# Kernel optimization log

Hardware: AMD Instinct MI355X
Metric: run time of the kernel (lower is better)

The kernel has to match this reference:

```python
import jax, jax.numpy as jnp
import numpy as np

EPS = 1e-6  # F.pairwise_distance default eps, added to the difference


def setup_inputs() -> dict:
    key = jax.random.key(0)
    k1, k2 = jax.random.split(key)
    N, NS, NQ, D = 2048, 5, 8, 256
    x = jax.random.normal(k1, (N, NS + NQ, D), dtype=jnp.float32)
    label = jax.random.randint(k2, (N,), 0, N, dtype=jnp.int64)
    return {"x": x, "label": label, "n_s": NS, "n_q": NQ}


def reference(x, label, n_s, n_q):
    # x: [N, n_s+n_q, D]
    anchors = jnp.mean(x[:, :n_s, :], axis=1)               # [N, D] prototypes
    N, D = anchors.shape
    queries = x[:, n_s:n_s + n_q, :].reshape(N * n_q, D)     # [N*n_q, D]

    # Exact ||q - a + eps||^2 via GEMM expansion (matches F.pairwise_distance(.,.)**2):
    # ||q-a||^2 + 2*eps*sum(q-a) + D*eps^2
    q_sq = jnp.sum(queries * queries, axis=-1)               # [N*n_q]
    a_sq = jnp.sum(anchors * anchors, axis=-1)               # [N]
    cross = queries @ anchors.T                              # [N*n_q, N]
    q_sum = jnp.sum(queries, axis=-1)                        # [N*n_q]
    a_sum = jnp.sum(anchors, axis=-1)                        # [N]
    dist_sq = (q_sq[:, None] + a_sq[None, :] - 2.0 * cross
               + 2.0 * EPS * (q_sum[:, None] - a_sum[None, :])
               + D * EPS * EPS)
    logits = -dist_sq                                        # [N*n_q, N]

    lab = jnp.repeat(label, n_q)                             # [N*n_q]
    logp = jax.nn.log_softmax(logits, axis=-1)
    nloss = -jnp.mean(jnp.take_along_axis(logp, lab[:, None], axis=1))
    prec1 = jnp.mean((jnp.argmax(logits, axis=-1) == lab).astype(jnp.float32)) * 100.0
    return nloss, prec1
```

## Files before the change

### kernel.cpp

```cpp
#include <hip/hip_runtime.h>
#include <math.h>

#define EPS  1e-6f
#define DD   256
#define NSUP 5
#define NQ   8
#define SEQ  13
#define L2E  1.44269504088896f
#define LN2  0.693147180559945f
#define NEP  2048
#define NROW 16384
#define NCOL 2048

typedef short bf16x8 __attribute__((ext_vector_type(8)));
typedef unsigned short u16x4 __attribute__((ext_vector_type(4)));
typedef float f32x4  __attribute__((ext_vector_type(4)));

__device__ __forceinline__ ushort f2bf(float f) {
  union { float f; unsigned u; } v; v.f = f;
  unsigned r = v.u + 0x7FFFu + ((v.u >> 16) & 1u);
  return (ushort)(r >> 16);
}
__device__ __forceinline__ float bf2f(short u) {
  union { unsigned u; float f; } v; v.u = ((unsigned)(unsigned short)u) << 16;
  return v.f;
}

__global__ __launch_bounds__(256) void proto_prep(
    const float* __restrict__ x, float* __restrict__ cb,
    ushort* __restrict__ Asw, ushort* __restrict__ Qsw,
    float* __restrict__ accum, int* __restrict__ fincount) {
  const int tid = threadIdx.x, g = tid >> 6, l = tid & 63;
  const int n = blockIdx.x * 4 + g;
  if (blockIdx.x == 0 && tid == 0) { accum[0] = 0.f; accum[1] = 0.f; fincount[0] = 0; }

  const float4* xr4 = (const float4*)(x + (size_t)n * SEQ * DD);

  const int d0   = l * 4;
  const int kk   = d0 >> 5, quad = (d0 >> 3) & 3, j = d0 & 7;
  const size_t chunk_d = (size_t)kk * 64 + (size_t)quad * 16;

  float4 a = {0.f, 0.f, 0.f, 0.f};
  #pragma unroll
  for (int s = 0; s < NSUP; ++s) {
    float4 v = xr4[s * 64 + l];
    a.x += v.x; a.y += v.y; a.z += v.z; a.w += v.w;
  }
  a.x *= 0.2f; a.y *= 0.2f; a.z *= 0.2f; a.w *= 0.2f;
  {
    const size_t idx = (((size_t)(n >> 4) * 8) * 64 + chunk_d + (n & 15)) * 8 + j;
    u16x4 o = {f2bf(a.x), f2bf(a.y), f2bf(a.z), f2bf(a.w)};
    *(u16x4*)(Asw + idx) = o;
  }
  float s1 = a.x + a.y + a.z + a.w;
  float s2 = a.x * a.x + a.y * a.y + a.z * a.z + a.w * a.w;
  #pragma unroll
  for (int off = 32; off; off >>= 1) {
    s1 += __shfl_xor(s1, off);
    s2 += __shfl_xor(s2, off);
  }
  if (l == 0) cb[n] = -L2E * (s2 - 2.f * EPS * s1);

  #pragma unroll
  for (int s = 0; s < NQ; ++s) {
    float4 q = xr4[(NSUP + s) * 64 + l];
    const int row = n * NQ + s;
    const size_t idx = (((size_t)(row >> 4) * 8) * 64 + chunk_d + (row & 15)) * 8 + j;
    u16x4 o = {f2bf(q.x), f2bf(q.y), f2bf(q.z), f2bf(q.w)};
    *(u16x4*)(Qsw + idx) = o;
  }
}

__global__ __launch_bounds__(1024, 4) void proto_main(
    const ushort* __restrict__ Qsw, const ushort* __restrict__ Asw,
    const float* __restrict__ cb, const int* __restrict__ label,
    float* __restrict__ accum, int* __restrict__ fincount,
    float* __restrict__ out) {
  const int tid  = threadIdx.x;
  const int wid  = tid >> 6, lane = tid & 63;
  const int quad = lane >> 4, lcol = lane & 15;
  const int rowg = wid & 1, colg = wid >> 1;
  const int r0   = blockIdx.x * 64;

  const bf16x8* qb = (const bf16x8*)Qsw;
  const bf16x8* bb = (const bf16x8*)Asw;

  __shared__ bf16x8 Bl[8][2][8][64];

  bf16x8 af[2][8];
  #pragma unroll
  for (int set = 0; set < 2; ++set) {
    const size_t base = ((size_t)(blockIdx.x * 4 + rowg * 2 + set) * 8) * 64 + lane;
    #pragma unroll
    for (int kk = 0; kk < 8; ++kk) af[set][kk] = qb[base + (size_t)kk * 64];
  }

  float m[2][4], s[2][4];
  int   bi[2][4];
  #pragma unroll
  for (int set = 0; set < 2; ++set)
    #pragma unroll
    for (int i = 0; i < 4; ++i) {
      m[set][i] = -1e30f; s[set][i] = 0.f; bi[set][i] = 0x7fffffff;
    }

  const int kk0 = rowg * 4;
  auto stage = [&](int tl, int b) {
    const int T = colg * 16 + tl;
    #pragma unroll
    for (int k2 = 0; k2 < 4; ++k2) {
      const int kk = kk0 + k2;
      const ushort* src = Asw + (((size_t)T * 8 + kk) * 64 + lane) * 8;
      __builtin_amdgcn_global_load_lds(
          (const __attribute__((address_space(1))) void*)src,
          (__attribute__((address_space(3))) void*)&Bl[colg][b][kk][0],
          16, 0, 0);
    }
  };

  auto compute = [&](int tl, int b) {
    f32x4 c0 = {0.f, 0.f, 0.f, 0.f}, c1 = {0.f, 0.f, 0.f, 0.f};
    #pragma unroll
    for (int kk = 0; kk < 8; ++kk) {
      bf16x8 bf = Bl[colg][b][kk][lane];
      c0 = __builtin_amdgcn_mfma_f32_16x16x32_bf16(af[0][kk], bf, c0, 0, 0, 0);
      c1 = __builtin_amdgcn_mfma_f32_16x16x32_bf16(af[1][kk], bf, c1, 0, 0, 0);
    }
    const int   colIdx = (colg * 16 + tl) * 16 + lcol;
    const float cbv    = cb[colIdx];
    #pragma unroll
    for (int set = 0; set < 2; ++set) {
      #pragma unroll
      for (int i = 0; i < 4; ++i) {
        float cv = set ? c1[i] : c0[i];
        float v2 = fmaf(cv, 2.f * L2E, cbv);
        float dv = v2 - m[set][i];
        bool  gt = dv > 0.f;
        float e  = exp2f(-fabsf(dv));
        s[set][i]  = fmaf(s[set][i], gt ? e : 1.f, gt ? 1.f : e);
        m[set][i]  = fmaxf(m[set][i], v2);
        bi[set][i] = gt ? colIdx : bi[set][i];
      }
    }
  };

  stage(0, 0);
  __syncthreads();

  #pragma unroll 1
  for (int t = 0; t < 16; t += 2) {
    stage(t + 1, 1);
    compute(t, 0);
    __syncthreads();
    if (t + 2 < 16) stage(t + 2, 0);
    compute(t + 1, 1);
    __syncthreads();
  }

  #pragma unroll
  for (int mask = 1; mask < 16; mask <<= 1) {
    #pragma unroll
    for (int set = 0; set < 2; ++set)
      #pragma unroll
      for (int i = 0; i < 4; ++i) {
        float om = __shfl_xor(m[set][i], mask);
        float os = __shfl_xor(s[set][i], mask);
        int   oi = __shfl_xor(bi[set][i], mask);
        float nm = fmaxf(m[set][i], om);
        s[set][i] = s[set][i] * exp2f(m[set][i] - nm) + os * exp2f(om - nm);
        bool better = (om > m[set][i]) || (om == m[set][i] && oi < bi[set][i]);
        bi[set][i] = better ? oi : bi[set][i];
        m[set][i]  = nm;
      }
  }

  __shared__ float sm[8][64], ssh[8][64], slab[64];
  __shared__ int   sbi[8][64];
  if (lcol == 0) {
    #pragma unroll
    for (int set = 0; set < 2; ++set)
      #pragma unroll
      for (int i = 0; i < 4; ++i) {
        int rl = rowg * 32 + set * 16 + quad * 4 + i;
        sm[colg][rl] = m[set][i]; ssh[colg][rl] = s[set][i]; sbi[colg][rl] = bi[set][i];
      }
  }

  if (tid < 512) {
    const int rl = tid >> 3, l = tid & 7;
    const int row = r0 + rl;
    const int lab = label[row >> 3];
    const int kk  = l;
    float dot = 0.f;
    const size_t qc = ((size_t)(row >> 4) * 8 + kk) * 64 + (row & 15);
    const size_t ac = ((size_t)(lab >> 4) * 8 + kk) * 64 + (lab & 15);
    #pragma unroll
    for (int qd = 0; qd < 4; ++qd) {
      bf16x8 qv = qb[qc + qd * 16];
      bf16x8 av = bb[ac + qd * 16];
      #pragma unroll
      for (int j = 0; j < 8; ++j) dot = fmaf(bf2f(qv[j]), bf2f(av[j]), dot);
    }
    dot += __shfl_xor(dot, 1);
    dot += __shfl_xor(dot, 2);
    dot += __shfl_xor(dot, 4);
    if (l == 0) slab[rl] = fmaf(dot, 2.f * L2E, cb[lab]);
  }
  __syncthreads();

  if (tid < 64) {
    float mm = sm[0][tid], sv = ssh[0][tid];
    int   b  = sbi[0][tid];
    #pragma unroll
    for (int w = 1; w < 8; ++w) {
      float om = sm[w][tid], os = ssh[w][tid];
      int   oi = sbi[w][tid];
      float nm = fmaxf(mm, om);
      sv = sv * exp2f(mm - nm) + os * exp2f(om - nm);
      bool better = (om > mm) || (om == mm && oi < b);
      b = better ? oi : b;
      mm = nm;
    }
    const int row = r0 + tid;
    const int lb  = label[row >> 3];
    float loss = LN2 * (mm + log2f(sv) - slab[tid]);
    float corr = (b == lb) ? 1.f : 0.f;
    #pragma unroll
    for (int mask = 32; mask; mask >>= 1) {
      loss += __shfl_xor(loss, mask);
      corr += __shfl_xor(corr, mask);
    }
    if (tid == 0) {
      atomicAdd(&accum[0], loss);
      atomicAdd(&accum[1], corr);
      __threadfence();
      if (atomicAdd(fincount, 1) == (int)gridDim.x - 1) {
        out[0] = atomicAdd(&accum[0], 0.f) / (float)NROW;
        out[1] = atomicAdd(&accum[1], 0.f) * 100.f / (float)NROW;
      }
    }
  }
}

extern "C" void kernel_launch(void* const* d_in, const int* in_sizes, int n_in,
                              void* d_out, int out_size, void* d_ws, size_t ws_size,
                              hipStream_t stream) {
  const float* x     = (const float*)d_in[0];
  const int*   label = (const int*)d_in[1];
  float* out = (float*)d_out;

  float*  W        = (float*)d_ws;
  float*  accum    = W;
  int*    fincount = (int*)(W + 2);
  float*  cb       = W + 16;
  ushort* Asw      = (ushort*)(cb + NCOL);
  ushort* Qsw      = Asw + (size_t)NCOL * DD;

  hipLaunchKernelGGL(proto_prep, dim3(NEP / 4), dim3(256), 0, stream,
                     x, cb, Asw, Qsw, accum, fincount);
  hipLaunchKernelGGL(proto_main, dim3(NROW / 64), dim3(1024), 0, stream,
                     Qsw, Asw, cb, label, accum, fincount, out);
}
```

Baseline: 121.8 us.

## Software-pipeline MFMA tiles against online softmax and cache column bias in LDS

The per-tile loop is restructured so the MFMA accumulation for tile t runs while the online softmax/argmax update for tile t-1 executes, with two sets of accumulators alternating. The column bias vector is also copied once into shared memory, so the per-tile bias reads come from LDS rather than global memory. This aims to hide the exp/compare latency behind matrix work. In exchange it holds more live accumulator registers and adds 8KB of LDS per block, which could reduce occupancy under the 1024-thread, 4-block launch bound.

```diff
diff --git a/kernel.cpp b/kernel.cpp
--- a/kernel.cpp
+++ b/kernel.cpp
@@ -86,6 +86,10 @@
   const bf16x8* bb = (const bf16x8*)Asw;
 
   __shared__ bf16x8 Bl[8][2][8][64];
+  __shared__ float  sCb[NCOL];
+
+  sCb[tid]        = cb[tid];
+  sCb[tid + 1024] = cb[tid + 1024];
 
   bf16x8 af[2][8];
   #pragma unroll
@@ -118,22 +122,26 @@
     }
   };
 
-  auto compute = [&](int tl, int b) {
-    f32x4 c0 = {0.f, 0.f, 0.f, 0.f}, c1 = {0.f, 0.f, 0.f, 0.f};
+  auto mfmaT = [&](int tl, f32x4 (&c)[2]) {
+    c[0] = f32x4{0.f, 0.f, 0.f, 0.f};
+    c[1] = f32x4{0.f, 0.f, 0.f, 0.f};
+    const int b = tl & 1;
     #pragma unroll
     for (int kk = 0; kk < 8; ++kk) {
       bf16x8 bf = Bl[colg][b][kk][lane];
-      c0 = __builtin_amdgcn_mfma_f32_16x16x32_bf16(af[0][kk], bf, c0, 0, 0, 0);
-      c1 = __builtin_amdgcn_mfma_f32_16x16x32_bf16(af[1][kk], bf, c1, 0, 0, 0);
-    }
+      c[0] = __builtin_amdgcn_mfma_f32_16x16x32_bf16(af[0][kk], bf, c[0], 0, 0, 0);
+      c[1] = __builtin_amdgcn_mfma_f32_16x16x32_bf16(af[1][kk], bf, c[1], 0, 0, 0);
+    }
+  };
+
+  auto smax = [&](int tl, f32x4 (&c)[2]) {
     const int   colIdx = (colg * 16 + tl) * 16 + lcol;
-    const float cbv    = cb[colIdx];
+    const float cbv    = sCb[colIdx];
     #pragma unroll
     for (int set = 0; set < 2; ++set) {
       #pragma unroll
       for (int i = 0; i < 4; ++i) {
-        float cv = set ? c1[i] : c0[i];
-        float v2 = fmaf(cv, 2.f * L2E, cbv);
+        float v2 = fmaf(c[set][i], 2.f * L2E, cbv);
         float dv = v2 - m[set][i];
         bool  gt = dv > 0.f;
         float e  = exp2f(-fabsf(dv));
@@ -144,18 +152,28 @@
     }
   };
 
+  f32x4 cE[2], cO[2];
+
   stage(0, 0);
   __syncthreads();
+  stage(1, 1);
+  mfmaT(0, cE);
+  __syncthreads();
 
   #pragma unroll 1
-  for (int t = 0; t < 16; t += 2) {
-    stage(t + 1, 1);
-    compute(t, 0);
+  for (int t = 1; t < 15; t += 2) {
+    stage(t + 1, 0);
+    mfmaT(t, cO);
+    smax(t - 1, cE);
     __syncthreads();
-    if (t + 2 < 16) stage(t + 2, 0);
-    compute(t + 1, 1);
+    stage(t + 2, 1);
+    mfmaT(t + 1, cE);
+    smax(t, cO);
     __syncthreads();
   }
+  mfmaT(15, cO);
+  smax(14, cE);
+  smax(15, cO);
 
   #pragma unroll
   for (int mask = 1; mask < 16; mask <<= 1) {
@@ -204,7 +222,7 @@
     dot += __shfl_xor(dot, 1);
     dot += __shfl_xor(dot, 2);
     dot += __shfl_xor(dot, 4);
-    if (l == 0) slab[rl] = fmaf(dot, 2.f * L2E, cb[lab]);
+    if (l == 0) slab[rl] = fmaf(dot, 2.f * L2E, sCb[lab]);
   }
   __syncthreads();
 
```

New measurement: 126.7 us. +4.0%, slower.

## Split GEMM columns across two blocks with 128-row tiles and add merge kernel

Applied to the files above, without the earlier changes.

The main kernel now handles 128 query rows per block, with 4 row groups by 4 column groups, and covers half of the 2048 prototype columns. This keeps the grid at 256 blocks while each staged B tile is reused across twice as many rows. Per-half softmax partials (max, sum, argmax) and the label logits are written to workspace, and a new third kernel merges the two halves and reduces loss and accuracy. The column bias is also cached in shared memory. The cost is an extra launch, a global round trip for the partials, and fewer columns per block to amortize the Q fragment loads.

```diff
diff --git a/kernel.cpp b/kernel.cpp
--- a/kernel.cpp
+++ b/kernel.cpp
@@ -74,23 +74,28 @@
 __global__ __launch_bounds__(1024, 4) void proto_main(
     const ushort* __restrict__ Qsw, const ushort* __restrict__ Asw,
     const float* __restrict__ cb, const int* __restrict__ label,
-    float* __restrict__ accum, int* __restrict__ fincount,
-    float* __restrict__ out) {
+    float* __restrict__ partm, float* __restrict__ parts,
+    int* __restrict__ partbi, float* __restrict__ slabws) {
   const int tid  = threadIdx.x;
   const int wid  = tid >> 6, lane = tid & 63;
   const int quad = lane >> 4, lcol = lane & 15;
-  const int rowg = wid & 1, colg = wid >> 1;
-  const int r0   = blockIdx.x * 64;
+  const int rowg = wid & 3, colg = wid >> 2;
+  const int rb   = blockIdx.x >> 1;
+  const int colc = blockIdx.x & 1;
+  const int r0   = rb * 128;
 
   const bf16x8* qb = (const bf16x8*)Qsw;
   const bf16x8* bb = (const bf16x8*)Asw;
 
-  __shared__ bf16x8 Bl[8][2][8][64];
+  __shared__ bf16x8 Bl[4][2][8][64];
+  __shared__ float  sCb[1024];
+
+  sCb[tid] = cb[colc * 1024 + tid];
 
   bf16x8 af[2][8];
   #pragma unroll
   for (int set = 0; set < 2; ++set) {
-    const size_t base = ((size_t)(blockIdx.x * 4 + rowg * 2 + set) * 8) * 64 + lane;
+    const size_t base = ((size_t)(rb * 8 + rowg * 2 + set) * 8) * 64 + lane;
     #pragma unroll
     for (int kk = 0; kk < 8; ++kk) af[set][kk] = qb[base + (size_t)kk * 64];
   }
@@ -104,11 +109,11 @@
       m[set][i] = -1e30f; s[set][i] = 0.f; bi[set][i] = 0x7fffffff;
     }
 
-  const int kk0 = rowg * 4;
+  const int kk0 = rowg * 2;
   auto stage = [&](int tl, int b) {
-    const int T = colg * 16 + tl;
-    #pragma unroll
-    for (int k2 = 0; k2 < 4; ++k2) {
+    const int T = colc * 64 + colg * 16 + tl;
+    #pragma unroll
+    for (int k2 = 0; k2 < 2; ++k2) {
       const int kk = kk0 + k2;
       const ushort* src = Asw + (((size_t)T * 8 + kk) * 64 + lane) * 8;
       __builtin_amdgcn_global_load_lds(
@@ -126,8 +131,9 @@
       c0 = __builtin_amdgcn_mfma_f32_16x16x32_bf16(af[0][kk], bf, c0, 0, 0, 0);
       c1 = __builtin_amdgcn_mfma_f32_16x16x32_bf16(af[1][kk], bf, c1, 0, 0, 0);
     }
-    const int   colIdx = (colg * 16 + tl) * 16 + lcol;
-    const float cbv    = cb[colIdx];
+    const int   lcIdx  = (colg * 16 + tl) * 16 + lcol;
+    const int   colIdx = colc * 1024 + lcIdx;
+    const float cbv    = sCb[lcIdx];
     #pragma unroll
     for (int set = 0; set < 2; ++set) {
       #pragma unroll
@@ -174,8 +180,8 @@
       }
   }
 
-  __shared__ float sm[8][64], ssh[8][64], slab[64];
-  __shared__ int   sbi[8][64];
+  __shared__ float sm[4][128], ssh[4][128];
+  __shared__ int   sbi[4][128];
   if (lcol == 0) {
     #pragma unroll
     for (int set = 0; set < 2; ++set)
@@ -185,8 +191,28 @@
         sm[colg][rl] = m[set][i]; ssh[colg][rl] = s[set][i]; sbi[colg][rl] = bi[set][i];
       }
   }
-
-  if (tid < 512) {
+  __syncthreads();
+
+  if (tid < 128) {
+    float mm = sm[0][tid], sv = ssh[0][tid];
+    int   b  = sbi[0][tid];
+    #pragma unroll
+    for (int w = 1; w < 4; ++w) {
+      float om = sm[w][tid], os = ssh[w][tid];
+      int   oi = sbi[w][tid];
+      float nm = fmaxf(mm, om);
+      sv = sv * exp2f(mm - nm) + os * exp2f(om - nm);
+      bool better = (om > mm) || (om == mm && oi < b);
+      b = better ? oi : b;
+      mm = nm;
+    }
+    const int row = r0 + tid;
+    partm [colc * NROW + row] = mm;
+    parts [colc * NROW + row] = sv;
+    partbi[colc * NROW + row] = b;
+  }
+
+  if (colc == 0) {
     const int rl = tid >> 3, l = tid & 7;
     const int row = r0 + rl;
     const int lab = label[row >> 3];
@@ -204,40 +230,48 @@
     dot += __shfl_xor(dot, 1);
     dot += __shfl_xor(dot, 2);
     dot += __shfl_xor(dot, 4);
-    if (l == 0) slab[rl] = fmaf(dot, 2.f * L2E, cb[lab]);
-  }
+    if (l == 0) slabws[row] = fmaf(dot, 2.f * L2E, cb[lab]);
+  }
+}
+
+__global__ __launch_bounds__(256) void proto_merge(
+    const float* __restrict__ partm, const float* __restrict__ parts,
+    const int* __restrict__ partbi, const float* __restrict__ slabws,
+    const int* __restrict__ label,
+    float* __restrict__ accum, int* __restrict__ fincount,
+    float* __restrict__ out) {
+  const int tid = threadIdx.x, row = blockIdx.x * 256 + tid;
+  const int wid = tid >> 6;
+
+  float m0 = partm[row],  m1 = partm[NROW + row];
+  float s0 = parts[row],  s1 = parts[NROW + row];
+  int   b0 = partbi[row], b1 = partbi[NROW + row];
+  float nm = fmaxf(m0, m1);
+  float sv = s0 * exp2f(m0 - nm) + s1 * exp2f(m1 - nm);
+  bool better = (m1 > m0) || (m1 == m0 && b1 < b0);
+  int  b  = better ? b1 : b0;
+
+  const int lb = label[row >> 3];
+  float loss = LN2 * (nm + log2f(sv) - slabws[row]);
+  float corr = (b == lb) ? 1.f : 0.f;
+
+  #pragma unroll
+  for (int mask = 32; mask; mask >>= 1) {
+    loss += __shfl_xor(loss, mask);
+    corr += __shfl_xor(corr, mask);
+  }
+  __shared__ float red[2][4];
+  if ((tid & 63) == 0) { red[0][wid] = loss; red[1][wid] = corr; }
   __syncthreads();
-
-  if (tid < 64) {
-    float mm = sm[0][tid], sv = ssh[0][tid];
-    int   b  = sbi[0][tid];
-    #pragma unroll
-    for (int w = 1; w < 8; ++w) {
-      float om = sm[w][tid], os = ssh[w][tid];
-      int   oi = sbi[w][tid];
-      float nm = fmaxf(mm, om);
-      sv = sv * exp2f(mm - nm) + os * exp2f(om - nm);
-      bool better = (om > mm) || (om == mm && oi < b);
-      b = better ? oi : b;
-      mm = nm;
-    }
-    const int row = r0 + tid;
-    const int lb  = label[row >> 3];
-    float loss = LN2 * (mm + log2f(sv) - slab[tid]);
-    float corr = (b == lb) ? 1.f : 0.f;
-    #pragma unroll
-    for (int mask = 32; mask; mask >>= 1) {
-      loss += __shfl_xor(loss, mask);
-      corr += __shfl_xor(corr, mask);
-    }
-    if (tid == 0) {
-      atomicAdd(&accum[0], loss);
-      atomicAdd(&accum[1], corr);
-      __threadfence();
-      if (atomicAdd(fincount, 1) == (int)gridDim.x - 1) {
-        out[0] = atomicAdd(&accum[0], 0.f) / (float)NROW;
-        out[1] = atomicAdd(&accum[1], 0.f) * 100.f / (float)NROW;
-      }
+  if (tid == 0) {
+    float L = red[0][0] + red[0][1] + red[0][2] + red[0][3];
+    float C = red[1][0] + red[1][1] + red[1][2] + red[1][3];
+    atomicAdd(&accum[0], L);
+    atomicAdd(&accum[1], C);
+    __threadfence();
+    if (atomicAdd(fincount, 1) == (int)gridDim.x - 1) {
+      out[0] = atomicAdd(&accum[0], 0.f) / (float)NROW;
+      out[1] = atomicAdd(&accum[1], 0.f) * 100.f / (float)NROW;
     }
   }
 }
@@ -255,9 +289,15 @@
   float*  cb       = W + 16;
   ushort* Asw      = (ushort*)(cb + NCOL);
   ushort* Qsw      = Asw + (size_t)NCOL * DD;
+  float*  partm    = (float*)(Qsw + (size_t)NROW * DD);
+  float*  parts    = partm + 2 * NROW;
+  int*    partbi   = (int*)(parts + 2 * NROW);
+  float*  slabws   = (float*)(partbi + 2 * NROW);
 
   hipLaunchKernelGGL(proto_prep, dim3(NEP / 4), dim3(256), 0, stream,
                      x, cb, Asw, Qsw, accum, fincount);
-  hipLaunchKernelGGL(proto_main, dim3(NROW / 64), dim3(1024), 0, stream,
-                     Qsw, Asw, cb, label, accum, fincount, out);
-}
+  hipLaunchKernelGGL(proto_main, dim3(256), dim3(1024), 0, stream,
+                     Qsw, Asw, cb, label, partm, parts, partbi, slabws);
+  hipLaunchKernelGGL(proto_merge, dim3(NROW / 256), dim3(256), 0, stream,
+                     partm, parts, partbi, slabws, label, accum, fincount, out);
+}
```

Result: faster. 119.0 us (-2.3%).
